# Kernel tuning notes

Measured on AMD Instinct MI355X. Metric: run time of the kernel, lower is better.

Reference implementation:

```python
import jax, jax.numpy as jnp
import numpy as np

B, C, N, HID = 1, 64, 1024, 128


def setup_inputs() -> dict:
    key = jax.random.key(0)
    k1, k2, k3, k4, k5 = jax.random.split(key, 5)
    x = jax.random.normal(k1, (B, C, N), dtype=jnp.float32)
    # Conv2d(2C -> HID, 1): weight [HID, 2C] (1x1 kernel flattened), bias [HID]
    W1 = jax.random.normal(k2, (HID, 2 * C), dtype=jnp.float32) * (1.0 / np.sqrt(2 * C))
    b1 = jax.random.normal(k3, (HID,), dtype=jnp.float32) * 0.01
    # Conv2d(HID -> 1, 1): weight [HID], bias [1]
    W2 = jax.random.normal(k4, (HID,), dtype=jnp.float32) * (1.0 / np.sqrt(HID))
    b2 = jax.random.normal(k5, (1,), dtype=jnp.float32) * 0.01
    return {"x": x, "W1": W1, "b1": b1, "W2": W2, "b2": b2}


def reference(x, W1, b1, W2, b2):
    # Original: m1[b,c,i,j] = x[b,c,j]; m2[b,c,i,j] = x[b,c,i]; block = cat([m1, m2], dim=1)
    # tanh is elementwise, and the 1x1 conv is linear, so we split W1 into the
    # halves acting on m1 (j-indexed) and m2 (i-indexed) and avoid the explicit
    # O(N^2 * 2C) repeat+concat. The nonlinear hidden tensor [B,HID,N,N] is the
    # same math as Conv2d(tanh(block)).
    c = x.shape[1]
    t = jnp.tanh(x)                                   # [B, C, N]
    pj = jnp.einsum('hc,bcn->bhn', W1[:, :c], t)      # contribution of m1 (varies over j)
    pi = jnp.einsum('hc,bcn->bhn', W1[:, c:], t)      # contribution of m2 (varies over i)
    h = jnp.tanh(pi[:, :, :, None] + pj[:, :, None, :] + b1[None, :, None, None])  # [B,HID,N,N]
    e = jnp.einsum('h,bhij->bij', W2, h) + b2[0]      # [B, N, N]
    return e + jnp.swapaxes(e, 1, 2)
```

## Files before the change

kernel.cpp:

```cpp
#include <hip/hip_runtime.h>
#include <math.h>

#define CN    64
#define NN    1024
#define NPAIR 528

__device__ __forceinline__ float tanh_fast(float x) {
    float e = __expf(2.0f * x);
    return 1.0f - 2.0f * __builtin_amdgcn_rcpf(e + 1.0f);
}

__global__ __launch_bounds__(256) void prep_kernel(
    const float* __restrict__ x, const float* __restrict__ W1,
    const float* __restrict__ b1, float2* __restrict__ S)
{
    __shared__ float t_s[2][64];
    const int tid = threadIdx.x;
    const int n0  = blockIdx.x * 2;

    if (tid < 64) {
        float2 xv = *(const float2*)&x[tid * NN + n0];
        t_s[0][tid] = tanh_fast(xv.x);
        t_s[1][tid] = tanh_fast(xv.y);
    }
    __syncthreads();

    const int h  = tid & 127;
    const int nl = tid >> 7;
    const float4* wrow = (const float4*)(W1 + h * (2 * CN));

    float pj[4] = {0.f, 0.f, 0.f, 0.f};
    float pi[4] = {0.f, 0.f, 0.f, 0.f};
#pragma unroll
    for (int c4 = 0; c4 < 16; ++c4) {
        float4 tv = *(const float4*)&t_s[nl][c4 * 4];
        float4 wl = wrow[c4];
        float4 wh = wrow[16 + c4];
        const int s = c4 & 3;
        pj[s] = fmaf(wl.x, tv.x, fmaf(wl.y, tv.y, fmaf(wl.z, tv.z, fmaf(wl.w, tv.w, pj[s]))));
        pi[s] = fmaf(wh.x, tv.x, fmaf(wh.y, tv.y, fmaf(wh.z, tv.z, fmaf(wh.w, tv.w, pi[s]))));
    }
    float pjs = (pj[0] + pj[1]) + (pj[2] + pj[3]);
    float pis = (pi[0] + pi[1]) + (pi[2] + pi[3]);
    float U = tanh_fast(pis + b1[h]);
    float V = tanh_fast(pjs);
    S[h * NN + n0 + nl] = make_float2(U, V);
}

__global__ __launch_bounds__(256) void pair_kernel(
    const float2* __restrict__ S, const float* __restrict__ W2,
    const float* __restrict__ b2, float* __restrict__ out)
{
    const int pair = blockIdx.x;
    int r = (int)((sqrtf(8.f * pair + 1.f) - 1.f) * 0.5f);
    while ((r + 1) * (r + 2) / 2 <= pair) ++r;
    while (r * (r + 1) / 2 > pair) --r;
    const int bi = pair - r * (r + 1) / 2, bj = r;
    const int i0 = bi * 32, j0 = bj * 32;

    __shared__ float4 sm4[4096];
    const int tid = threadIdx.x;

    {
        const float4* SF = (const float4*)S;
        const int ci = i0 >> 1, cj = j0 >> 1;
#pragma unroll
        for (int k = 0; k < 8; ++k) {
            int idx = k * 256 + tid;
            int h = idx >> 4, seg = idx & 15;
            sm4[idx]        = SF[h * 512 + ci + seg];
            sm4[2048 + idx] = SF[h * 512 + cj + seg];
        }
    }
    __syncthreads();

    const int w = tid >> 6, lane = tid & 63;
    const int la = lane & 7, lb = lane >> 3;
    const float2* Si = (const float2*)sm4;
    const float2* Sj = (const float2*)(sm4 + 2048);

    float acc[16];
#pragma unroll
    for (int q = 0; q < 16; ++q) acc[q] = 0.f;

    const int hbase = w * 32;
#pragma unroll 4
    for (int hh = 0; hh < 32; ++hh) {
        const int h = hbase + hh;
        const float w2h = W2[h];
        float2 A[4], B[4];
        float PA[4], QA[4], PB[4], QB[4];
#pragma unroll
        for (int m = 0; m < 4; ++m) {
            A[m]  = Si[h * 32 + la + 8 * m];
            PA[m] = w2h * (A[m].x + A[m].y);
            QA[m] = fmaf(A[m].x, A[m].y, 1.0f);
        }
#pragma unroll
        for (int n = 0; n < 4; ++n) {
            B[n]  = Sj[h * 32 + lb + 8 * n];
            PB[n] = w2h * (B[n].x + B[n].y);
            QB[n] = fmaf(B[n].x, B[n].y, 1.0f);
        }
#pragma unroll
        for (int m = 0; m < 4; ++m)
#pragma unroll
            for (int n = 0; n < 4; ++n) {
                float d1 = fmaf(A[m].x, B[n].y, 1.0f);
                float d2 = fmaf(B[n].x, A[m].y, 1.0f);
                float rr = __builtin_amdgcn_rcpf(d1 * d2);
                float Np = fmaf(PB[n], QA[m], PA[m] * QB[n]);
                acc[m * 4 + n] = fmaf(Np, rr, acc[m * 4 + n]);
            }
    }

    __syncthreads();
    float* buf = (float*)sm4;
#pragma unroll
    for (int q = 0; q < 16; ++q)
        buf[w * 1024 + q * 64 + lane] = acc[q];
    __syncthreads();

    float* T = (float*)(sm4 + 1024);
    const float bias2 = 2.0f * b2[0];
#pragma unroll
    for (int k = 0; k < 4; ++k) {
        int c  = tid + k * 256;
        int q  = c >> 6, l2 = c & 63;
        int m = q >> 2, n = q & 3;
        int il = (l2 & 7) + 8 * m, jl = (l2 >> 3) + 8 * n;
        float v = buf[c] + buf[1024 + c] + buf[2048 + c] + buf[3072 + c] + bias2;
        T[il * 34 + jl] = v;
    }
    __syncthreads();

    const int tx = tid & 15, ty = tid >> 4;
#pragma unroll
    for (int k = 0; k < 4; ++k) {
        int rr2 = ty + (k >> 1) * 16;
        int cc2 = tx + (k & 1) * 16;
        out[(i0 + rr2) * NN + j0 + cc2] = T[rr2 * 34 + cc2];
    }
    if (bi != bj) {
#pragma unroll
        for (int k = 0; k < 4; ++k) {
            int rr2 = ty + (k >> 1) * 16;
            int cc2 = tx + (k & 1) * 16;
            out[(j0 + rr2) * NN + i0 + cc2] = T[cc2 * 34 + rr2];
        }
    }
}

extern "C" void kernel_launch(void* const* d_in, const int* in_sizes, int n_in,
                              void* d_out, int out_size, void* d_ws, size_t ws_size,
                              hipStream_t stream)
{
    const float* x  = (const float*)d_in[0];
    const float* W1 = (const float*)d_in[1];
    const float* b1 = (const float*)d_in[2];
    const float* W2 = (const float*)d_in[3];
    const float* b2 = (const float*)d_in[4];
    float* out = (float*)d_out;
    float2* S  = (float2*)d_ws;

    prep_kernel<<<512, 256, 0, stream>>>(x, W1, b1, S);
    pair_kernel<<<NPAIR, 256, 0, stream>>>(S, W2, b2, out);
}
```

Measured before the change: 95.66 us.

## Pair hidden units to share reciprocals and exploit symmetry in diagonal tiles

The hidden-unit data is re-laid out so each float4 holds two hidden units, and the per-cell tanh-sum terms for two units are combined over a common denominator. This halves the reciprocal count per cell. Diagonal tiles are merged two per block and compute only the upper triangle, giving exactly 512 blocks of 512 threads. The cost is extra multiplies per cell, more shared-memory reduction across eight waves, and more complex index bookkeeping that could hide errors.

```diff
diff --git a/kernel.cpp b/kernel.cpp
--- a/kernel.cpp
+++ b/kernel.cpp
@@ -3,7 +3,7 @@
 
 #define CN    64
 #define NN    1024
-#define NPAIR 528
+#define NOFF  496
 
 __device__ __forceinline__ float tanh_fast(float x) {
     float e = __expf(2.0f * x);
@@ -12,7 +12,7 @@
 
 __global__ __launch_bounds__(256) void prep_kernel(
     const float* __restrict__ x, const float* __restrict__ W1,
-    const float* __restrict__ b1, float2* __restrict__ S)
+    const float* __restrict__ b1, float2* __restrict__ S2h)
 {
     __shared__ float t_s[2][64];
     const int tid = threadIdx.x;
@@ -44,109 +44,182 @@
     float pis = (pi[0] + pi[1]) + (pi[2] + pi[3]);
     float U = tanh_fast(pis + b1[h]);
     float V = tanh_fast(pjs);
-    S[h * NN + n0 + nl] = make_float2(U, V);
-}
-
-__global__ __launch_bounds__(256) void pair_kernel(
-    const float2* __restrict__ S, const float* __restrict__ W2,
+    S2h[(((h >> 1) * NN) + n0 + nl) * 2 + (h & 1)] = make_float2(U, V);
+}
+
+__device__ __forceinline__ void cell_term(
+    const float4& A, const float4& B,
+    float PAe, float QAe, float PAo, float QAo,
+    float pBe, float qBe, float pBo, float qBo, float& a)
+{
+    float d1e = fmaf(A.x, B.y, 1.f);
+    float d2e = fmaf(B.x, A.y, 1.f);
+    float De  = d1e * d2e;
+    float Ne  = fmaf(PAe, qBe, pBe * QAe);
+    float d1o = fmaf(A.z, B.w, 1.f);
+    float d2o = fmaf(B.z, A.w, 1.f);
+    float Do  = d1o * d2o;
+    float No  = fmaf(PAo, qBo, pBo * QAo);
+    float Num = fmaf(Ne, Do, No * De);
+    a = fmaf(Num, __builtin_amdgcn_rcpf(De * Do), a);
+}
+
+template<bool DIAG>
+__device__ __forceinline__ void run_chunk(
+    const float4* __restrict__ Abase, const float4* __restrict__ Bbase,
+    const float2* __restrict__ W2p, int hp0, int hp1,
+    int la, int lb, float* acc)
+{
+#pragma unroll 2
+    for (int hp = hp0; hp < hp1; ++hp) {
+        const float2 w2 = W2p[hp];
+        float4 A[4], B[4];
+        float PAe[4], QAe[4], PAo[4], QAo[4];
+        float pBe[4], qBe[4], pBo[4], qBo[4];
+#pragma unroll
+        for (int m = 0; m < 4; ++m) {
+            A[m]   = Abase[hp * 32 + la + 8 * m];
+            PAe[m] = w2.x * (A[m].x + A[m].y);
+            QAe[m] = w2.x * fmaf(A[m].x, A[m].y, 1.f);
+            PAo[m] = w2.y * (A[m].z + A[m].w);
+            QAo[m] = w2.y * fmaf(A[m].z, A[m].w, 1.f);
+        }
+#pragma unroll
+        for (int n = 0; n < 4; ++n) {
+            B[n]   = Bbase[hp * 32 + lb + 8 * n];
+            pBe[n] = B[n].x + B[n].y;
+            qBe[n] = fmaf(B[n].x, B[n].y, 1.f);
+            pBo[n] = B[n].z + B[n].w;
+            qBo[n] = fmaf(B[n].z, B[n].w, 1.f);
+        }
+        if (DIAG) {
+            int idx = 0;
+#pragma unroll
+            for (int m = 0; m < 4; ++m)
+#pragma unroll
+                for (int n = 0; n < 4; ++n)
+                    if (n >= m)
+                        cell_term(A[m], B[n], PAe[m], QAe[m], PAo[m], QAo[m],
+                                  pBe[n], qBe[n], pBo[n], qBo[n], acc[idx++]);
+        } else {
+#pragma unroll
+            for (int m = 0; m < 4; ++m)
+#pragma unroll
+                for (int n = 0; n < 4; ++n)
+                    cell_term(A[m], B[n], PAe[m], QAe[m], PAo[m], QAo[m],
+                              pBe[n], qBe[n], pBo[n], qBo[n], acc[m * 4 + n]);
+        }
+    }
+}
+
+__global__ __launch_bounds__(512, 4) void pair_kernel(
+    const float4* __restrict__ S2, const float* __restrict__ W2,
     const float* __restrict__ b2, float* __restrict__ out)
 {
-    const int pair = blockIdx.x;
-    int r = (int)((sqrtf(8.f * pair + 1.f) - 1.f) * 0.5f);
-    while ((r + 1) * (r + 2) / 2 <= pair) ++r;
-    while (r * (r + 1) / 2 > pair) --r;
-    const int bi = pair - r * (r + 1) / 2, bj = r;
-    const int i0 = bi * 32, j0 = bj * 32;
-
-    __shared__ float4 sm4[4096];
+    const int id  = blockIdx.x;
     const int tid = threadIdx.x;
-
+    const bool dual = (id < 16);
+
+    int i0, j0;
+    if (dual) {
+        i0 = (2 * id) * 32; j0 = (2 * id + 1) * 32;
+    } else {
+        int p = id - 16;
+        int r = (int)((1.f + sqrtf(8.f * p + 1.f)) * 0.5f);
+        while (r * (r - 1) / 2 > p) --r;
+        while (r * (r + 1) / 2 <= p) ++r;
+        int c = p - r * (r - 1) / 2;
+        i0 = c * 32; j0 = r * 32;
+    }
+
+    __shared__ float4 sm[4096];
     {
-        const float4* SF = (const float4*)S;
-        const int ci = i0 >> 1, cj = j0 >> 1;
-#pragma unroll
-        for (int k = 0; k < 8; ++k) {
-            int idx = k * 256 + tid;
-            int h = idx >> 4, seg = idx & 15;
-            sm4[idx]        = SF[h * 512 + ci + seg];
-            sm4[2048 + idx] = SF[h * 512 + cj + seg];
+#pragma unroll
+        for (int k = 0; k < 4; ++k) {
+            int idx = k * 512 + tid;
+            int hp = idx >> 5, seg = idx & 31;
+            sm[idx]        = S2[hp * NN + i0 + seg];
+            sm[2048 + idx] = S2[hp * NN + j0 + seg];
         }
     }
     __syncthreads();
 
     const int w = tid >> 6, lane = tid & 63;
     const int la = lane & 7, lb = lane >> 3;
-    const float2* Si = (const float2*)sm4;
-    const float2* Sj = (const float2*)(sm4 + 2048);
+    const float4* SiF = sm;
+    const float4* SjF = sm + 2048;
+    const float2* W2p = (const float2*)W2;
 
     float acc[16];
 #pragma unroll
     for (int q = 0; q < 16; ++q) acc[q] = 0.f;
 
-    const int hbase = w * 32;
-#pragma unroll 4
-    for (int hh = 0; hh < 32; ++hh) {
-        const int h = hbase + hh;
-        const float w2h = W2[h];
-        float2 A[4], B[4];
-        float PA[4], QA[4], PB[4], QB[4];
-#pragma unroll
-        for (int m = 0; m < 4; ++m) {
-            A[m]  = Si[h * 32 + la + 8 * m];
-            PA[m] = w2h * (A[m].x + A[m].y);
-            QA[m] = fmaf(A[m].x, A[m].y, 1.0f);
-        }
-#pragma unroll
-        for (int n = 0; n < 4; ++n) {
-            B[n]  = Sj[h * 32 + lb + 8 * n];
-            PB[n] = w2h * (B[n].x + B[n].y);
-            QB[n] = fmaf(B[n].x, B[n].y, 1.0f);
-        }
-#pragma unroll
-        for (int m = 0; m < 4; ++m)
-#pragma unroll
-            for (int n = 0; n < 4; ++n) {
-                float d1 = fmaf(A[m].x, B[n].y, 1.0f);
-                float d2 = fmaf(B[n].x, A[m].y, 1.0f);
-                float rr = __builtin_amdgcn_rcpf(d1 * d2);
-                float Np = fmaf(PB[n], QA[m], PA[m] * QB[n]);
-                acc[m * 4 + n] = fmaf(Np, rr, acc[m * 4 + n]);
-            }
+    if (dual) {
+        const float4* base = (w < 4) ? SiF : SjF;
+        const int hp0 = (w & 3) * 16;
+        run_chunk<true>(base, base, W2p, hp0, hp0 + 16, la, lb, acc);
+    } else {
+        run_chunk<false>(SiF, SjF, W2p, 8 * w, 8 * w + 8, la, lb, acc);
     }
 
     __syncthreads();
-    float* buf = (float*)sm4;
-#pragma unroll
-    for (int q = 0; q < 16; ++q)
-        buf[w * 1024 + q * 64 + lane] = acc[q];
-    __syncthreads();
-
-    float* T = (float*)(sm4 + 1024);
+    float* buf = (float*)sm;
     const float bias2 = 2.0f * b2[0];
-#pragma unroll
-    for (int k = 0; k < 4; ++k) {
-        int c  = tid + k * 256;
-        int q  = c >> 6, l2 = c & 63;
-        int m = q >> 2, n = q & 3;
-        int il = (l2 & 7) + 8 * m, jl = (l2 >> 3) + 8 * n;
-        float v = buf[c] + buf[1024 + c] + buf[2048 + c] + buf[3072 + c] + bias2;
-        T[il * 34 + jl] = v;
-    }
-    __syncthreads();
-
-    const int tx = tid & 15, ty = tid >> 4;
-#pragma unroll
-    for (int k = 0; k < 4; ++k) {
-        int rr2 = ty + (k >> 1) * 16;
-        int cc2 = tx + (k & 1) * 16;
-        out[(i0 + rr2) * NN + j0 + cc2] = T[rr2 * 34 + cc2];
-    }
-    if (bi != bj) {
-#pragma unroll
-        for (int k = 0; k < 4; ++k) {
-            int rr2 = ty + (k >> 1) * 16;
-            int cc2 = tx + (k & 1) * 16;
-            out[(j0 + rr2) * NN + i0 + cc2] = T[cc2 * 34 + rr2];
+
+    if (!dual) {
+#pragma unroll
+        for (int q = 0; q < 16; ++q)
+            buf[w * 1024 + q * 64 + lane] = acc[q];
+        __syncthreads();
+
+        float* T = (float*)sm + 8192;
+        for (int c = tid; c < 1024; c += 512) {
+            float v = bias2;
+#pragma unroll
+            for (int wv = 0; wv < 8; ++wv) v += buf[wv * 1024 + c];
+            int q = c >> 6, l2 = c & 63;
+            int m = q >> 2, n = q & 3;
+            T[((l2 & 7) + 8 * m) * 34 + (l2 >> 3) + 8 * n] = v;
+        }
+        __syncthreads();
+
+        const int tx = tid & 31, ty = tid >> 5;
+        out[(i0 + ty)      * NN + j0 + tx] = T[ty * 34 + tx];
+        out[(i0 + ty + 16) * NN + j0 + tx] = T[(ty + 16) * 34 + tx];
+        out[(j0 + ty)      * NN + i0 + tx] = T[tx * 34 + ty];
+        out[(j0 + ty + 16) * NN + i0 + tx] = T[tx * 34 + ty + 16];
+    } else {
+#pragma unroll
+        for (int q = 0; q < 10; ++q)
+            buf[w * 640 + q * 64 + lane] = acc[q];
+        __syncthreads();
+
+        float* T0 = (float*)sm + 6144;
+        float* T1 = (float*)sm + 7296;
+        for (int c = tid; c < 1280; c += 512) {
+            int s = (c >= 640) ? 1 : 0;
+            int cc = c - 640 * s;
+            float v = bias2;
+#pragma unroll
+            for (int wv = 0; wv < 4; ++wv) v += buf[(s * 4 + wv) * 640 + cc];
+            int qq = cc >> 6, l2 = cc & 63;
+            int m = (qq >= 4) + (qq >= 7) + (qq >= 9);
+            int start = (m == 0) ? 0 : (m == 1) ? 4 : (m == 2) ? 7 : 9;
+            int n = qq - start + m;
+            int il = (l2 & 7) + 8 * m, jl = (l2 >> 3) + 8 * n;
+            float* T = s ? T1 : T0;
+            T[il * 34 + jl] = v;
+            if (m != n) T[jl * 34 + il] = v;
+        }
+        __syncthreads();
+
+        const int tx = tid & 31, ty = tid >> 5;
+#pragma unroll
+        for (int s = 0; s < 2; ++s) {
+            const float* T = s ? T1 : T0;
+            const int b0 = s ? j0 : i0;
+            out[(b0 + ty)      * NN + b0 + tx] = T[ty * 34 + tx];
+            out[(b0 + ty + 16) * NN + b0 + tx] = T[(ty + 16) * 34 + tx];
         }
     }
 }
@@ -161,8 +234,8 @@
     const float* W2 = (const float*)d_in[3];
     const float* b2 = (const float*)d_in[4];
     float* out = (float*)d_out;
-    float2* S  = (float2*)d_ws;
-
-    prep_kernel<<<512, 256, 0, stream>>>(x, W1, b1, S);
-    pair_kernel<<<NPAIR, 256, 0, stream>>>(S, W2, b2, out);
-}
+
+    float2* S2h = (float2*)d_ws;
+    prep_kernel<<<512, 256, 0, stream>>>(x, W1, b1, S2h);
+    pair_kernel<<<512, 512, 0, stream>>>((const float4*)d_ws, W2, b2, out);
+}
```

New measurement: 90.12 us. -5.8%, faster.
